# Performance work log

Measured on AMD Instinct MI355X. Metric: run time of the kernel, lower is better.

## Reference

```python
import jax, jax.numpy as jnp
import numpy as np

N_NODES, N_EDGES, IN_DIM, H, D = 50000, 800000, 256, 4, 32
NEG_SLOPE = 0.2  # DGL GATv2Conv default


def setup_inputs() -> dict:
    key = jax.random.key(0)
    k = jax.random.split(key, 7)
    s_in = 1.0 / np.sqrt(IN_DIM)
    return {
        "h": jax.random.normal(k[0], (N_NODES, IN_DIM), jnp.float32),
        "src": jax.random.randint(k[1], (N_EDGES,), 0, N_NODES, jnp.int32),
        "dst": jax.random.randint(k[2], (N_EDGES,), 0, N_NODES, jnp.int32),
        "W_src": jax.random.normal(k[3], (IN_DIM, H * D), jnp.float32) * s_in,
        "b_src": jnp.zeros((H * D,), jnp.float32),
        "W_dst": jax.random.normal(k[4], (IN_DIM, H * D), jnp.float32) * s_in,
        "b_dst": jnp.zeros((H * D,), jnp.float32),
        "attn_a": jax.random.normal(k[5], (H, D), jnp.float32) * 0.1,
    }


def reference(h, src, dst, W_src, b_src, W_dst, b_dst, attn_a):
    """GATv2Conv (hop=1, get_attention=True) + reshape, as in TweetEmbedder.forward."""
    N = h.shape[0]
    el = (h @ W_src + b_src).reshape(N, H, D)  # fc_src, per-head
    er = (h @ W_dst + b_dst).reshape(N, H, D)  # fc_dst, per-head
    # edge scores: e_ij = a^T leaky_relu(W_src h_i + W_dst h_j)
    e = jax.nn.leaky_relu(el[src] + er[dst], NEG_SLOPE)          # (E, H, D)
    scores = jnp.einsum('ehd,hd->eh', e, attn_a)                  # (E, H)
    # edge softmax over incoming edges of each dst node
    m = jax.ops.segment_max(scores, dst, num_segments=N)          # (N, H)
    ex = jnp.exp(scores - m[dst])
    denom = jax.ops.segment_sum(ex, dst, num_segments=N)          # (N, H)
    a = ex / denom[dst]                                           # (E, H)
    # weighted scatter-aggregate of source messages
    out = jax.ops.segment_sum(a[:, :, None] * el[src], dst, num_segments=N)  # (N, H, D)
    return out.reshape(N, H * D), a[:, :, None]
```

## Files before the change

### kernel.cpp

```cpp
#include <hip/hip_runtime.h>
#include <cstdint>
#include <cstddef>

#define NNODES 50000
#define NEDGES 800000
#define INDIM  256
#define HD     128
#define NH     4
#define NEG    0.2f
#define LOG2E  1.44269504088896340736f

#define PAD    16

#define SCAN_B ((NNODES + 255) / 256)

#define CLR_BLKS   ((NNODES * PAD / 4 + 255) / 256)
#define CONVW_BLKS 64
#define GEMM_BLKS  ((NNODES + 127) / 128)
#define HIST_BLKS  ((NEDGES + 2047) / 2048)
#define SCAT_BLKS  ((NEDGES + 2047) / 2048)

typedef __attribute__((ext_vector_type(8))) short   short8;
typedef __attribute__((ext_vector_type(8))) ushort  ushort8;
typedef __attribute__((ext_vector_type(4))) float   floatx4;

#define EXP2(x) __builtin_amdgcn_exp2f(x)

__device__ __forceinline__ ushort f2bf(float f) {
    unsigned u = __float_as_uint(f);
    unsigned r = u + 0x7fffu + ((u >> 16) & 1u);
    return (ushort)(r >> 16);
}
__device__ __forceinline__ float bf2f(ushort u) {
    return __uint_as_float(((unsigned)u) << 16);
}

__device__ __forceinline__ int swz(int c) { return c ^ ((c >> 4) & 7); }

__global__ __launch_bounds__(256) void fusedPre_kernel(
        int* __restrict__ cnt_work,
        const float* __restrict__ Wsrc, const float* __restrict__ Wdst,
        ushort* __restrict__ Wt) {
    __shared__ float t[32][33];
    const int bid = blockIdx.x;
    const int tid = threadIdx.x;

    if (bid < CLR_BLKS) {
        int i = bid * 256 + tid;
        if (i < NNODES * PAD / 4)
            ((int4*)cnt_work)[i] = make_int4(0, 0, 0, 0);
        return;
    }
    int wb = bid - CLR_BLKS;
    int kb = (wb & 7) * 32, nb = (wb >> 3) * 32;
    int tx = tid & 31, ty = tid >> 5;
    for (int i = ty; i < 32; i += 8) {
        int k = kb + i, n = nb + tx;
        float v = (n < HD) ? Wsrc[(size_t)k * HD + n] : Wdst[(size_t)k * HD + (n - HD)];
        t[i][tx] = v;
    }
    __syncthreads();
    for (int i = ty; i < 32; i += 8) {
        int n = nb + i, k = kb + tx;
        Wt[(size_t)n * INDIM + k] = f2bf(t[tx][i]);
    }
}

__global__ __launch_bounds__(256, 2) void fusedG_kernel(
        const float* __restrict__ h, const ushort* __restrict__ Wt,
        const float* __restrict__ bsrc, const float* __restrict__ bdst,
        ushort* __restrict__ el_bf, float* __restrict__ er,
        const int* __restrict__ dst, int* __restrict__ cnt_work) {
    __shared__ ushort As[512 * 8];
    __shared__ ushort Bs[1024 * 8];

    const int bid = blockIdx.x;
    const int tid = threadIdx.x;

    if (bid >= GEMM_BLKS) {
        int base = (bid - GEMM_BLKS) * 2048 + tid;
        int dd[8];
#pragma unroll
        for (int k = 0; k < 8; ++k) {
            int e = base + k * 256;
            dd[k] = (e < NEDGES) ? dst[e] : -1;
        }
#pragma unroll
        for (int k = 0; k < 8; ++k) {
            if (dd[k] >= 0) atomicAdd(cnt_work + (size_t)dd[k] * PAD, 1);
        }
        return;
    }

    const int wave = tid >> 6, lane = tid & 63;
    const int row0 = bid * 128;
    const int l15  = lane & 15, quad = lane >> 4;

    floatx4 acc[2][16];
#pragma unroll
    for (int i = 0; i < 2; ++i)
#pragma unroll
        for (int j = 0; j < 16; ++j) acc[i][j] = (floatx4){0.f, 0.f, 0.f, 0.f};

    for (int kk = 0; kk < INDIM; kk += 32) {
#pragma unroll
        for (int it = 0; it < 2; ++it) {
            int idx = tid + it * 256;
            int r = idx >> 2;
            int kq = idx & 3;
            int c = (r >> 4) * 64 + kq * 16 + (r & 15);
            int grow = row0 + r;
            ushort8 aw = (ushort8){0,0,0,0,0,0,0,0};
            if (grow < NNODES) {
                const float* p = h + (size_t)grow * INDIM + kk + kq * 8;
                float4 v0 = *(const float4*)p;
                float4 v1 = *(const float4*)(p + 4);
                aw[0] = f2bf(v0.x); aw[1] = f2bf(v0.y); aw[2] = f2bf(v0.z); aw[3] = f2bf(v0.w);
                aw[4] = f2bf(v1.x); aw[5] = f2bf(v1.y); aw[6] = f2bf(v1.z); aw[7] = f2bf(v1.w);
            }
            *(ushort8*)(As + swz(c) * 8) = aw;
        }
#pragma unroll
        for (int it = 0; it < 4; ++it) {
            int idx = tid + it * 256;
            int r = idx >> 2;
            int kq = idx & 3;
            int c = (r >> 4) * 64 + kq * 16 + (r & 15);
            ushort8 bw = *(const ushort8*)(Wt + (size_t)r * INDIM + kk + kq * 8);
            *(ushort8*)(Bs + swz(c) * 8) = bw;
        }
        __syncthreads();

        short8 af[2];
#pragma unroll
        for (int tm = 0; tm < 2; ++tm) {
            int c = (wave * 2 + tm) * 64 + quad * 16 + l15;
            af[tm] = *(const short8*)(As + swz(c) * 8);
        }
#pragma unroll
        for (int tn = 0; tn < 16; ++tn) {
            int c = tn * 64 + quad * 16 + l15;
            short8 bfr = *(const short8*)(Bs + swz(c) * 8);
            acc[0][tn] = __builtin_amdgcn_mfma_f32_16x16x32_bf16(af[0], bfr, acc[0][tn], 0, 0, 0);
            acc[1][tn] = __builtin_amdgcn_mfma_f32_16x16x32_bf16(af[1], bfr, acc[1][tn], 0, 0, 0);
        }
        __syncthreads();
    }

#pragma unroll
    for (int tn = 0; tn < 8; ++tn) {
        int col = tn * 16 + l15;
        float bias = bsrc[col];
#pragma unroll
        for (int tm = 0; tm < 2; ++tm)
#pragma unroll
            for (int reg = 0; reg < 4; ++reg) {
                int row = row0 + wave * 32 + tm * 16 + quad * 4 + reg;
                if (row < NNODES)
                    el_bf[(size_t)row * HD + col] = f2bf(acc[tm][tn][reg] + bias);
            }
    }
#pragma unroll
    for (int tn = 8; tn < 16; ++tn) {
        int col = tn * 16 + l15 - HD;
        float bias = bdst[col];
#pragma unroll
        for (int tm = 0; tm < 2; ++tm)
#pragma unroll
            for (int reg = 0; reg < 4; ++reg) {
                int row = row0 + wave * 32 + tm * 16 + quad * 4 + reg;
                if (row < NNODES)
                    er[(size_t)row * HD + col] = acc[tm][tn][reg] + bias;
            }
    }
}

__global__ __launch_bounds__(256) void scan_partial_kernel(
        const int* __restrict__ cnt, int* __restrict__ partials) {
    __shared__ int lds[256];
    int i = blockIdx.x * 256 + threadIdx.x;
    lds[threadIdx.x] = (i < NNODES) ? cnt[(size_t)i * PAD] : 0;
    __syncthreads();
    for (int off = 128; off > 0; off >>= 1) {
        if (threadIdx.x < off) lds[threadIdx.x] += lds[threadIdx.x + off];
        __syncthreads();
    }
    if (threadIdx.x == 0) partials[blockIdx.x] = lds[0];
}

__global__ __launch_bounds__(256) void scan_final_kernel(
        int* __restrict__ cnt_work, const int* __restrict__ partials,
        int* __restrict__ rowptr) {
    __shared__ int lds[256];
    __shared__ int sh_prefix;
    const int t = threadIdx.x;
    const int bid = blockIdx.x;

    int pv = (t < bid) ? partials[t] : 0;
    lds[t] = pv;
    __syncthreads();
    for (int off = 128; off > 0; off >>= 1) {
        if (t < off) lds[t] += lds[t + off];
        __syncthreads();
    }
    if (t == 0) sh_prefix = lds[0];
    __syncthreads();
    const int prefix = sh_prefix;
    __syncthreads();

    const int i = bid * 256 + t;
    int v = (i < NNODES) ? cnt_work[(size_t)i * PAD] : 0;
    lds[t] = v;
    __syncthreads();
    for (int off = 1; off < 256; off <<= 1) {
        int u = (t >= off) ? lds[t - off] : 0;
        __syncthreads();
        lds[t] += u;
        __syncthreads();
    }
    if (i < NNODES) {
        int start = prefix + lds[t] - v;
        rowptr[i] = start;
        cnt_work[(size_t)i * PAD] = start;
    }
    if (bid == SCAN_B - 1 && t == 255) rowptr[NNODES] = prefix + lds[255];
}

__global__ __launch_bounds__(256) void scatter_kernel(
        const int* __restrict__ src, const int* __restrict__ dst,
        int* __restrict__ cnt_work, int2* __restrict__ epair) {
    int base = blockIdx.x * 2048 + threadIdx.x;
    int ss[8], dd[8], pos[8];
#pragma unroll
    for (int k = 0; k < 8; ++k) {
        int e = base + k * 256;
        if (e < NEDGES) { ss[k] = src[e]; dd[k] = dst[e]; } else dd[k] = -1;
    }
#pragma unroll
    for (int k = 0; k < 8; ++k) {
        if (dd[k] >= 0) pos[k] = atomicAdd(cnt_work + (size_t)dd[k] * PAD, 1);
    }
#pragma unroll
    for (int k = 0; k < 8; ++k) {
        int e = base + k * 256;
        if (dd[k] >= 0) epair[pos[k]] = make_int2(e, ss[k]);
    }
}

#define DEGCAP 128

__global__ __launch_bounds__(256) void node_fused_kernel(
        const ushort* __restrict__ el_bf, float* __restrict__ erout,
        const int* __restrict__ rowptr, const int2* __restrict__ epair,
        const float* __restrict__ attn, float* __restrict__ out_a) {
    __shared__ float sp[4][DEGCAP * NH];

    const int wv = threadIdx.x >> 6;
    const int n = blockIdx.x * 4 + wv;
    if (n >= NNODES) return;
    const int lane = threadIdx.x & 63;
    const int hh = lane >> 4;
    const int lo = rowptr[n], hi = rowptr[n + 1];
    const int deg = hi - lo;
    float* spw = sp[wv];
    const int l2 = lane * 2;

    const float2 rv = *(const float2*)(erout + (size_t)n * HD + l2);
    const float a0 = attn[l2] * LOG2E, a1 = attn[l2 + 1] * LOG2E;

    float m = -3.4e38f, lsum = 0.0f, acc0 = 0.0f, acc1 = 0.0f;

    if (deg > 0 && deg <= DEGCAP) {
        int jj0 = (lane & 15);
        if (jj0 >= deg) jj0 = deg - 1;
        int si = epair[lo + jj0].y;

        for (int base = 0; base < deg; base += 16) {
            ushort2 u[16];
#pragma unroll
            for (int j = 0; j < 16; ++j) {
                if (base + j < deg) {
                    int s = __builtin_amdgcn_readlane(si, j);
                    u[j] = *(const ushort2*)(el_bf + (size_t)s * HD + l2);
                }
            }
            int si_nxt = si;
            if (base + 16 < deg) {
                int jj = base + 16 + (lane & 15);
                if (jj >= deg) jj = deg - 1;
                si_nxt = epair[lo + jj].y;
            }
#pragma unroll
            for (int j = 0; j < 16; ++j) {
                if (base + j < deg) {
                    float evx = bf2f(u[j].x), evy = bf2f(u[j].y);
                    float x0 = evx + rv.x; x0 = fmaxf(x0, NEG * x0);
                    float x1 = evy + rv.y; x1 = fmaxf(x1, NEG * x1);
                    float p = x0 * a0 + x1 * a1;
                    p += __shfl_xor(p, 1, 16);
                    p += __shfl_xor(p, 2, 16);
                    p += __shfl_xor(p, 4, 16);
                    p += __shfl_xor(p, 8, 16);
                    if ((lane & 15) == 0) spw[(base + j) * NH + hh] = p;
                    float mn = fmaxf(m, p);
                    float sc = EXP2(m - mn);
                    float w  = EXP2(p - mn);
                    lsum = lsum * sc + w;
                    acc0 = acc0 * sc + w * evx;
                    acc1 = acc1 * sc + w * evy;
                    m = mn;
                }
            }
            si = si_nxt;
        }
    } else if (deg > DEGCAP) {
        ushort2 u = {0,0};
        { int s_ = epair[lo].y; u = *(const ushort2*)(el_bf + (size_t)s_ * HD + l2); }
        for (int i = lo; i < hi; ++i) {
            float evx = bf2f(u.x), evy = bf2f(u.y);
            if (i + 1 < hi) { int s_ = epair[i + 1].y;
                u = *(const ushort2*)(el_bf + (size_t)s_ * HD + l2); }
            float x0 = evx + rv.x; x0 = fmaxf(x0, NEG * x0);
            float x1 = evy + rv.y; x1 = fmaxf(x1, NEG * x1);
            float p = x0 * a0 + x1 * a1;
            p += __shfl_xor(p, 1, 16);
            p += __shfl_xor(p, 2, 16);
            p += __shfl_xor(p, 4, 16);
            p += __shfl_xor(p, 8, 16);
            float mn = fmaxf(m, p);
            float sc = EXP2(m - mn);
            float w  = EXP2(p - mn);
            lsum = lsum * sc + w;
            acc0 = acc0 * sc + w * evx;
            acc1 = acc1 * sc + w * evy;
            m = mn;
        }
    }

    float2 o;
    if (deg == 0) { o.x = 0.0f; o.y = 0.0f; }
    else { float inv = 1.0f / lsum; o.x = acc0 * inv; o.y = acc1 * inv; }
    *(float2*)(erout + (size_t)n * HD + l2) = o;

    if (deg == 0) return;

    float inv = 1.0f / lsum;
    if (deg <= DEGCAP) {
        float mh   = __shfl(m,   (lane & 3) << 4, 64);
        float invh = __shfl(inv, (lane & 3) << 4, 64);
        for (int q = (lane >> 2); q < deg; q += 16) {
            int e = epair[lo + q].x;
            float p = spw[q * NH + (lane & 3)];
            out_a[(size_t)e * NH + (lane & 3)] = EXP2(p - mh) * invh;
        }
    } else {
        for (int i = lo; i < hi; ++i) {
            int s_ = epair[i].y;
            ushort2 u = *(const ushort2*)(el_bf + (size_t)s_ * HD + l2);
            float evx = bf2f(u.x), evy = bf2f(u.y);
            float x0 = evx + rv.x; x0 = fmaxf(x0, NEG * x0);
            float x1 = evy + rv.y; x1 = fmaxf(x1, NEG * x1);
            float p = x0 * a0 + x1 * a1;
            p += __shfl_xor(p, 1, 16);
            p += __shfl_xor(p, 2, 16);
            p += __shfl_xor(p, 4, 16);
            p += __shfl_xor(p, 8, 16);
            if ((lane & 15) == 0) {
                int e = epair[i].x;
                out_a[(size_t)e * NH + hh] = EXP2(p - m) * inv;
            }
        }
    }
}

extern "C" void kernel_launch(void* const* d_in, const int* in_sizes, int n_in,
                              void* d_out, int out_size, void* d_ws, size_t ws_size,
                              hipStream_t stream) {
    const float* h    = (const float*)d_in[0];
    const int*   src  = (const int*)d_in[1];
    const int*   dst  = (const int*)d_in[2];
    const float* Wsrc = (const float*)d_in[3];
    const float* bsrc = (const float*)d_in[4];
    const float* Wdst = (const float*)d_in[5];
    const float* bdst = (const float*)d_in[6];
    const float* attn = (const float*)d_in[7];

    float* out_feat = (float*)d_out;
    float* out_a    = out_feat + (size_t)NNODES * HD;

    ushort* Wt       = (ushort*)d_ws;
    ushort* el_bf    = Wt + 2 * HD * INDIM;
    int*    cnt_work = (int*)(el_bf + (size_t)NNODES * HD);
    int2*   epair    = (int2*)(cnt_work + (size_t)NNODES * PAD);
    int*    rowptr   = (int*)(epair + NEDGES);
    int*    partials = rowptr + NNODES + 1;

    fusedPre_kernel<<<CLR_BLKS + CONVW_BLKS, 256, 0, stream>>>(
        cnt_work, Wsrc, Wdst, Wt);

    fusedG_kernel<<<GEMM_BLKS + HIST_BLKS, 256, 0, stream>>>(
        h, Wt, bsrc, bdst, el_bf, out_feat, dst, cnt_work);

    scan_partial_kernel<<<SCAN_B, 256, 0, stream>>>(cnt_work, partials);
    scan_final_kernel<<<SCAN_B, 256, 0, stream>>>(cnt_work, partials, rowptr);

    scatter_kernel<<<SCAT_BLKS, 256, 0, stream>>>(src, dst, cnt_work, epair);

    node_fused_kernel<<<(NNODES + 3) / 4, 256, 0, stream>>>(
        el_bf, out_feat, rowptr, epair, attn, out_a);
}
```

Measured before the change: 267.1 us.

## Record per-edge rank in histogram pass and drop second atomic pass in scatter

The histogram pass now keeps the value returned by each atomicAdd as a per-edge rank. The scatter kernel then computes each position as rowptr[dst] + rank with no atomics, where before it ran a second round of atomics on the counters. The counter array is also made dense instead of padded to 16 ints per node, which shrinks the clear and the scan reads. The cost is an extra 3.2 MB rank array written and read, and dense counters can see more contention on shared cache lines during atomics.

```diff
diff --git a/kernel.cpp b/kernel.cpp
--- a/kernel.cpp
+++ b/kernel.cpp
@@ -10,14 +10,12 @@
 #define NEG    0.2f
 #define LOG2E  1.44269504088896340736f
 
-#define PAD    16
-
 #define SCAN_B ((NNODES + 255) / 256)
 
-#define CLR_BLKS   ((NNODES * PAD / 4 + 255) / 256)
+#define CLR_BLKS   49
 #define CONVW_BLKS 64
 #define GEMM_BLKS  ((NNODES + 127) / 128)
-#define HIST_BLKS  ((NEDGES + 2047) / 2048)
+#define RANK_BLKS  ((NEDGES + 2047) / 2048)
 #define SCAT_BLKS  ((NEDGES + 2047) / 2048)
 
 typedef __attribute__((ext_vector_type(8))) short   short8;
@@ -47,7 +45,7 @@
 
     if (bid < CLR_BLKS) {
         int i = bid * 256 + tid;
-        if (i < NNODES * PAD / 4)
+        if (i < (NNODES + 3) / 4)
             ((int4*)cnt_work)[i] = make_int4(0, 0, 0, 0);
         return;
     }
@@ -70,7 +68,8 @@
         const float* __restrict__ h, const ushort* __restrict__ Wt,
         const float* __restrict__ bsrc, const float* __restrict__ bdst,
         ushort* __restrict__ el_bf, float* __restrict__ er,
-        const int* __restrict__ dst, int* __restrict__ cnt_work) {
+        const int* __restrict__ dst, int* __restrict__ cnt_work,
+        int* __restrict__ rank) {
     __shared__ ushort As[512 * 8];
     __shared__ ushort Bs[1024 * 8];
 
@@ -79,7 +78,7 @@
 
     if (bid >= GEMM_BLKS) {
         int base = (bid - GEMM_BLKS) * 2048 + tid;
-        int dd[8];
+        int dd[8], pos[8];
 #pragma unroll
         for (int k = 0; k < 8; ++k) {
             int e = base + k * 256;
@@ -87,7 +86,12 @@
         }
 #pragma unroll
         for (int k = 0; k < 8; ++k) {
-            if (dd[k] >= 0) atomicAdd(cnt_work + (size_t)dd[k] * PAD, 1);
+            if (dd[k] >= 0) pos[k] = atomicAdd(cnt_work + dd[k], 1);
+        }
+#pragma unroll
+        for (int k = 0; k < 8; ++k) {
+            int e = base + k * 256;
+            if (dd[k] >= 0) rank[e] = pos[k];
         }
         return;
     }
@@ -179,7 +183,7 @@
         const int* __restrict__ cnt, int* __restrict__ partials) {
     __shared__ int lds[256];
     int i = blockIdx.x * 256 + threadIdx.x;
-    lds[threadIdx.x] = (i < NNODES) ? cnt[(size_t)i * PAD] : 0;
+    lds[threadIdx.x] = (i < NNODES) ? cnt[i] : 0;
     __syncthreads();
     for (int off = 128; off > 0; off >>= 1) {
         if (threadIdx.x < off) lds[threadIdx.x] += lds[threadIdx.x + off];
@@ -189,7 +193,7 @@
 }
 
 __global__ __launch_bounds__(256) void scan_final_kernel(
-        int* __restrict__ cnt_work, const int* __restrict__ partials,
+        const int* __restrict__ cnt_work, const int* __restrict__ partials,
         int* __restrict__ rowptr) {
     __shared__ int lds[256];
     __shared__ int sh_prefix;
@@ -209,7 +213,7 @@
     __syncthreads();
 
     const int i = bid * 256 + t;
-    int v = (i < NNODES) ? cnt_work[(size_t)i * PAD] : 0;
+    int v = (i < NNODES) ? cnt_work[i] : 0;
     lds[t] = v;
     __syncthreads();
     for (int off = 1; off < 256; off <<= 1) {
@@ -218,27 +222,27 @@
         lds[t] += u;
         __syncthreads();
     }
-    if (i < NNODES) {
-        int start = prefix + lds[t] - v;
-        rowptr[i] = start;
-        cnt_work[(size_t)i * PAD] = start;
-    }
+    if (i < NNODES)
+        rowptr[i] = prefix + lds[t] - v;
     if (bid == SCAN_B - 1 && t == 255) rowptr[NNODES] = prefix + lds[255];
 }
 
 __global__ __launch_bounds__(256) void scatter_kernel(
         const int* __restrict__ src, const int* __restrict__ dst,
-        int* __restrict__ cnt_work, int2* __restrict__ epair) {
+        const int* __restrict__ rank, const int* __restrict__ rowptr,
+        int2* __restrict__ epair) {
     int base = blockIdx.x * 2048 + threadIdx.x;
-    int ss[8], dd[8], pos[8];
+    int ss[8], dd[8], rk[8];
 #pragma unroll
     for (int k = 0; k < 8; ++k) {
         int e = base + k * 256;
-        if (e < NEDGES) { ss[k] = src[e]; dd[k] = dst[e]; } else dd[k] = -1;
-    }
+        if (e < NEDGES) { ss[k] = src[e]; dd[k] = dst[e]; rk[k] = rank[e]; }
+        else dd[k] = -1;
+    }
+    int pos[8];
 #pragma unroll
     for (int k = 0; k < 8; ++k) {
-        if (dd[k] >= 0) pos[k] = atomicAdd(cnt_work + (size_t)dd[k] * PAD, 1);
+        if (dd[k] >= 0) pos[k] = rowptr[dd[k]] + rk[k];
     }
 #pragma unroll
     for (int k = 0; k < 8; ++k) {
@@ -391,20 +395,21 @@
     ushort* Wt       = (ushort*)d_ws;
     ushort* el_bf    = Wt + 2 * HD * INDIM;
     int*    cnt_work = (int*)(el_bf + (size_t)NNODES * HD);
-    int2*   epair    = (int2*)(cnt_work + (size_t)NNODES * PAD);
+    int*    rank     = cnt_work + NNODES;
+    int2*   epair    = (int2*)(rank + NEDGES);
     int*    rowptr   = (int*)(epair + NEDGES);
     int*    partials = rowptr + NNODES + 1;
 
     fusedPre_kernel<<<CLR_BLKS + CONVW_BLKS, 256, 0, stream>>>(
         cnt_work, Wsrc, Wdst, Wt);
 
-    fusedG_kernel<<<GEMM_BLKS + HIST_BLKS, 256, 0, stream>>>(
-        h, Wt, bsrc, bdst, el_bf, out_feat, dst, cnt_work);
+    fusedG_kernel<<<GEMM_BLKS + RANK_BLKS, 256, 0, stream>>>(
+        h, Wt, bsrc, bdst, el_bf, out_feat, dst, cnt_work, rank);
 
     scan_partial_kernel<<<SCAN_B, 256, 0, stream>>>(cnt_work, partials);
     scan_final_kernel<<<SCAN_B, 256, 0, stream>>>(cnt_work, partials, rowptr);
 
-    scatter_kernel<<<SCAT_BLKS, 256, 0, stream>>>(src, dst, cnt_work, epair);
+    scatter_kernel<<<SCAT_BLKS, 256, 0, stream>>>(src, dst, rank, rowptr, epair);
 
     node_fused_kernel<<<(NNODES + 3) / 4, 256, 0, stream>>>(
         el_bf, out_feat, rowptr, epair, attn, out_a);
```

After: 237.0 us. -11.3%, faster.
